# Kernel tuning notes

Measured on AMD Instinct MI355X. Metric: run time of the kernel, lower is better.

The kernel has to match this reference:

```python
import jax, jax.numpy as jnp
import numpy as np

B, Q, N, C = 2, 1024, 4096, 768
H, D, REL = 12, 64, 32
SCALE = 1.0 / np.sqrt(D)


def _lin_coords(n_out, n_in):
    # align_corners=True mapping: x_in = x_out * (n_in-1)/(n_out-1)
    pos = jnp.arange(n_out, dtype=jnp.float32) * ((n_in - 1) / (n_out - 1))
    lo = jnp.clip(jnp.floor(pos).astype(jnp.int32), 0, n_in - 1)
    hi = jnp.clip(lo + 1, 0, n_in - 1)
    w = pos - lo.astype(jnp.float32)
    return lo, hi, w


def _interp_bias(bias, q_len, n_len):
    # bias: [H, 32, 32] -> [H, q_len, n_len] bilinear, align_corners=True
    lq, hq, wq = _lin_coords(q_len, REL)
    ln, hn, wn = _lin_coords(n_len, REL)
    b1 = bias[:, lq, :] * (1.0 - wq)[None, :, None] + bias[:, hq, :] * wq[None, :, None]  # [H,q,32]
    b2 = b1[:, :, ln] * (1.0 - wn)[None, None, :] + b1[:, :, hn] * wn[None, None, :]      # [H,q,n]
    return b2


def setup_inputs() -> dict:
    key = jax.random.key(0)
    ks = jax.random.split(key, 11)
    s = 1.0 / np.sqrt(C)
    return {
        "query": jax.random.normal(ks[0], (B, Q, C), jnp.float32),
        "key_value": jax.random.normal(ks[1], (B, N, C), jnp.float32),
        "Wq": jax.random.normal(ks[2], (C, C), jnp.float32) * s,
        "bq": jax.random.normal(ks[3], (C,), jnp.float32) * 0.01,
        "Wk": jax.random.normal(ks[4], (C, C), jnp.float32) * s,
        "bk": jax.random.normal(ks[5], (C,), jnp.float32) * 0.01,
        "Wv": jax.random.normal(ks[6], (C, C), jnp.float32) * s,
        "bv": jax.random.normal(ks[7], (C,), jnp.float32) * 0.01,
        "Wo": jax.random.normal(ks[8], (C, C), jnp.float32) * s,
        "bo": jax.random.normal(ks[9], (C,), jnp.float32) * 0.01,
        "rel_pos_bias": jax.random.normal(ks[10], (H, REL, REL), jnp.float32) * 0.02,
    }


def reference(query, key_value, Wq, bq, Wk, bk, Wv, bv, Wo, bo, rel_pos_bias):
    b, n, c = key_value.shape
    q_len = query.shape[1]
    # projections (dropout in eval mode -> identity)
    q = (query @ Wq + bq).reshape(b, q_len, H, D).transpose(0, 2, 1, 3)      # [B,H,Q,D]
    k = (key_value @ Wk + bk).reshape(b, n, H, D).transpose(0, 2, 1, 3)      # [B,H,N,D]
    v = (key_value @ Wv + bv).reshape(b, n, H, D).transpose(0, 2, 1, 3)      # [B,H,N,D]
    attn = jnp.einsum('bhqd,bhnd->bhqn', q, k) * SCALE
    attn = attn + _interp_bias(rel_pos_bias, q_len, n)[None]                 # [B,H,Q,N]
    p = jax.nn.softmax(attn, axis=-1)
    out = jnp.einsum('bhqn,bhnd->bhqd', p, v)
    out = out.transpose(0, 2, 1, 3).reshape(b, q_len, c)
    return out @ Wo + bo
```

## Files before the change

kernel.cpp:

```cpp
#include <hip/hip_runtime.h>
#include <stdint.h>

typedef unsigned short ushort_t;
typedef __bf16 bf16x8 __attribute__((ext_vector_type(8)));
typedef float f32x4 __attribute__((ext_vector_type(4)));
typedef unsigned short us4 __attribute__((ext_vector_type(4)));

#define LOG2E 1.4426950408889634f
#define NEG8L (-11.541560327111707f)
#define QSCALE 0.18033688011110974f

__device__ __forceinline__ ushort_t f2b(float f) {
    unsigned u = __float_as_uint(f);
    unsigned r = (u + 0x7fffu + ((u >> 16) & 1u)) >> 16;
    return (ushort_t)r;
}
__device__ __forceinline__ void gld16(const void* g, void* l) {
    __builtin_amdgcn_global_load_lds(
        (__attribute__((address_space(1))) void*)g,
        (__attribute__((address_space(3))) void*)l,
        16, 0, 0);
}

__global__ __launch_bounds__(256) void prep(
        const float* __restrict__ query, const float* __restrict__ keyv,
        const float* __restrict__ Wq, const float* __restrict__ Wk,
        const float* __restrict__ Wv, const float* __restrict__ Wo,
        const float* __restrict__ rel,
        ushort_t* __restrict__ qc, ushort_t* __restrict__ kvc,
        ushort_t* __restrict__ wtq, ushort_t* __restrict__ wtk,
        ushort_t* __restrict__ wtv, ushort_t* __restrict__ wto,
        ushort_t* __restrict__ b1b, ushort_t* __restrict__ wtab) {
    __shared__ ushort_t tsh[32][33];
    const int bid = blockIdx.x, tid = threadIdx.x;
    if (bid < 7680) {
        const float* src = (bid < 1536) ? query : keyv;
        ushort_t* dst = (bid < 1536) ? qc : kvc;
        int i = ((bid < 1536) ? bid : bid - 1536) * 256 + tid;
        float4 x = ((const float4*)src)[i];
        us4 v; v.x = f2b(x.x); v.y = f2b(x.y); v.z = f2b(x.z); v.w = f2b(x.w);
        ((us4*)dst)[i] = v;
    } else if (bid < 9984) {
        int t = bid - 7680, w = t / 576, tt = t - w * 576;
        const float* in = (w == 0) ? Wq : (w == 1) ? Wk : (w == 2) ? Wv : Wo;
        ushort_t* out = (w == 0) ? wtq : (w == 1) ? wtk : (w == 2) ? wtv : wto;
        int x = tid & 31, y = tid >> 5;
        int bx = (tt % 24) * 32, by = (tt / 24) * 32;
#pragma unroll
        for (int j = 0; j < 32; j += 8)
            tsh[y + j][x] = f2b(in[(size_t)(by + y + j) * 768 + bx + x]);
        __syncthreads();
#pragma unroll
        for (int j = 0; j < 32; j += 8)
            out[(size_t)(bx + y + j) * 768 + by + x] = tsh[x][y + j];
    } else if (bid < 11520) {
        int idx = (bid - 9984) * 256 + tid;
        int j = idx & 31, q = (idx >> 5) & 1023, h = idx >> 15;
        float pos = q * (31.0f / 1023.0f);
        float fl = floorf(pos);
        int lo = (int)fl; if (lo > 31) lo = 31;
        float w = pos - fl;
        int hi = lo + 1; if (hi > 31) hi = 31;
        float vlo = rel[(h * 32 + lo) * 32 + j];
        float vhi = rel[(h * 32 + hi) * 32 + j];
        b1b[idx] = f2b((vlo + (vhi - vlo) * w) * LOG2E);
    } else {
        int n = (bid - 11520) * 256 + tid;
        float pos = n * (31.0f / 4095.0f);
        float fl = floorf(pos);
        int ln = (int)fl; if (ln > 31) ln = 31;
        float wn = pos - fl;
        int hn = ln + 1; if (hn > 31) hn = 31;
        float vals[32];
#pragma unroll
        for (int j = 0; j < 32; ++j) vals[j] = 0.f;
        vals[ln] += 1.0f - wn;
        vals[hn] += wn;
#pragma unroll
        for (int j = 0; j < 32; ++j) wtab[n * 32 + j] = f2b(vals[j]);
    }
}

__device__ __forceinline__ void gemm_store(const float* __restrict__ bias,
                                           f32x4 a, void* out,
                                           int mode, int lsh, float scale,
                                           int mbase, int n) {
    if (mode == 2) {
        int h = n >> 6, d = n & 63;
        int b = mbase >> lsh, l = mbase & ((1 << lsh) - 1);
        float bvf = bias[n];
        us4 v;
        v.x = f2b((a[0] + bvf) * scale);
        v.y = f2b((a[1] + bvf) * scale);
        v.z = f2b((a[2] + bvf) * scale);
        v.w = f2b((a[3] + bvf) * scale);
        *(us4*)((ushort_t*)out + ((size_t)((b * 12 + h) * 64 + d) << lsh) + l) = v;
    } else if (mode == 3) {
        int h = mbase >> 6, dbase = mbase & 63;
        int b = n >> lsh, l = n & ((1 << lsh) - 1);
        us4 v;
        v.x = f2b((a[0] + bias[mbase + 0]) * scale);
        v.y = f2b((a[1] + bias[mbase + 1]) * scale);
        v.z = f2b((a[2] + bias[mbase + 2]) * scale);
        v.w = f2b((a[3] + bias[mbase + 3]) * scale);
        *(us4*)((ushort_t*)out + ((((size_t)(b * 12 + h) << lsh) + l) << 6) + dbase) = v;
    } else {
        float4 v;
        v.x = (a[0] + bias[mbase + 0]) * scale;
        v.y = (a[1] + bias[mbase + 1]) * scale;
        v.z = (a[2] + bias[mbase + 2]) * scale;
        v.w = (a[3] + bias[mbase + 3]) * scale;
        *(float4*)((float*)out + (size_t)n * 768 + mbase) = v;
    }
}

__device__ __forceinline__ void gemm_body128(const ushort_t* __restrict__ A,
                                             const ushort_t* __restrict__ Bt,
                                             const float* __restrict__ bias,
                                             void* __restrict__ out,
                                             int mode, int lsh, float scale,
                                             int m0, int n0,
                                             ushort_t* As, ushort_t* Bs, int tid) {
    const int wave = tid >> 6, lane = tid & 63;
    const int quad = lane >> 4, l15 = lane & 15;
    const int wm = wave >> 1, wn = wave & 1;
    const f32x4 z4 = {0.f, 0.f, 0.f, 0.f};
    f32x4 acc[4][4];
#pragma unroll
    for (int i = 0; i < 4; ++i)
#pragma unroll
        for (int j = 0; j < 4; ++j) acc[i][j] = z4;

    const int arow = lane >> 3;
    const int ablk = lane & 7;
    const int kswz = (ablk ^ arow) * 8;

    for (int kk = 0; kk < 768; kk += 64) {
        __syncthreads();
#pragma unroll
        for (int i = 0; i < 4; ++i) {
            int c = wave * 4 + i;
            gld16(A + (size_t)(m0 + c * 8 + arow) * 768 + kk + kswz, (void*)(As + c * 512));
            gld16(Bt + (size_t)(n0 + c * 8 + arow) * 768 + kk + kswz, (void*)(Bs + c * 512));
        }
        __syncthreads();
#pragma unroll
        for (int ks = 0; ks < 2; ++ks) {
            bf16x8 af[4], bf[4];
#pragma unroll
            for (int mb = 0; mb < 4; ++mb) {
                int r = wm * 64 + mb * 16 + l15;
                af[mb] = *(const bf16x8*)(As + r * 64 + (((ks * 4 + quad) ^ (r & 7)) * 8));
            }
#pragma unroll
            for (int nb = 0; nb < 4; ++nb) {
                int r = wn * 64 + nb * 16 + l15;
                bf[nb] = *(const bf16x8*)(Bs + r * 64 + (((ks * 4 + quad) ^ (r & 7)) * 8));
            }
#pragma unroll
            for (int mb = 0; mb < 4; ++mb)
#pragma unroll
                for (int nb = 0; nb < 4; ++nb)
                    acc[mb][nb] = __builtin_amdgcn_mfma_f32_16x16x32_bf16(af[mb], bf[nb], acc[mb][nb], 0, 0, 0);
        }
    }

#pragma unroll
    for (int mb = 0; mb < 4; ++mb) {
        int mbase = m0 + wm * 64 + mb * 16 + quad * 4;
#pragma unroll
        for (int nb = 0; nb < 4; ++nb) {
            int n = n0 + wn * 64 + nb * 16 + l15;
            gemm_store(bias, acc[mb][nb], out, mode, lsh, scale, mbase, n);
        }
    }
}

__device__ __forceinline__ void gemm_body64(const ushort_t* __restrict__ A,
                                            const ushort_t* __restrict__ Bt,
                                            const float* __restrict__ bias,
                                            void* __restrict__ out,
                                            int mode, int lsh, float scale,
                                            int m0, int n0,
                                            ushort_t* As, ushort_t* Bs, int tid) {
    const int wave = tid >> 6, lane = tid & 63;
    const int quad = lane >> 4, l15 = lane & 15;
    const f32x4 z4 = {0.f, 0.f, 0.f, 0.f};
    f32x4 acc[4];
#pragma unroll
    for (int j = 0; j < 4; ++j) acc[j] = z4;

    const int arow = lane >> 3;
    const int ablk = lane & 7;
    const int kswz = (ablk ^ arow) * 8;

    for (int kk = 0; kk < 768; kk += 64) {
        __syncthreads();
#pragma unroll
        for (int i = 0; i < 2; ++i) {
            int c = wave * 2 + i;
            gld16(A + (size_t)(m0 + c * 8 + arow) * 768 + kk + kswz, (void*)(As + c * 512));
            gld16(Bt + (size_t)(n0 + c * 8 + arow) * 768 + kk + kswz, (void*)(Bs + c * 512));
        }
        __syncthreads();
#pragma unroll
        for (int ks = 0; ks < 2; ++ks) {
            bf16x8 af, bf[4];
            {
                int r = wave * 16 + l15;
                af = *(const bf16x8*)(As + r * 64 + (((ks * 4 + quad) ^ (r & 7)) * 8));
            }
#pragma unroll
            for (int nb = 0; nb < 4; ++nb) {
                int r = nb * 16 + l15;
                bf[nb] = *(const bf16x8*)(Bs + r * 64 + (((ks * 4 + quad) ^ (r & 7)) * 8));
            }
#pragma unroll
            for (int nb = 0; nb < 4; ++nb)
                acc[nb] = __builtin_amdgcn_mfma_f32_16x16x32_bf16(af, bf[nb], acc[nb], 0, 0, 0);
        }
    }

    int mbase = m0 + wave * 16 + quad * 4;
#pragma unroll
    for (int nb = 0; nb < 4; ++nb) {
        int n = n0 + nb * 16 + l15;
        gemm_store(bias, acc[nb], out, mode, lsh, scale, mbase, n);
    }
}

__global__ __launch_bounds__(256) void proj3(const ushort_t* __restrict__ qc,
                                             const ushort_t* __restrict__ kvc,
                                             const ushort_t* __restrict__ wtq,
                                             const ushort_t* __restrict__ wtk,
                                             const ushort_t* __restrict__ wtv,
                                             const float* __restrict__ bq,
                                             const float* __restrict__ bk,
                                             const float* __restrict__ bv,
                                             ushort_t* __restrict__ qp,
                                             ushort_t* __restrict__ kp,
                                             ushort_t* __restrict__ vtp) {
    __shared__ __align__(16) ushort_t As[128 * 64];
    __shared__ __align__(16) ushort_t Bs[128 * 64];
    const int bid = blockIdx.x, tid = threadIdx.x;
    if (bid < 96) {
        int t = bid;
        int nt = (t & 7) + 8 * ((t >> 3) & 1), mt = t >> 4;
        gemm_body128(wtq, qc, bq, qp, 3, 10, QSCALE, mt * 128, nt * 128, As, Bs, tid);
    } else if (bid < 480) {
        int t = bid - 96;
        int nt = (t & 7) + 8 * ((t >> 3) & 7), mt = t >> 6;
        gemm_body128(wtk, kvc, bk, kp, 3, 12, 1.0f, mt * 128, nt * 128, As, Bs, tid);
    } else {
        int t = bid - 480, mt = t & 63, nt = t >> 6;
        gemm_body128(kvc, wtv, bv, vtp, 2, 12, 1.0f, mt * 128, nt * 128, As, Bs, tid);
    }
}

__global__ __launch_bounds__(256) void gemm_out(const ushort_t* __restrict__ ab,
                                                const ushort_t* __restrict__ wto,
                                                const float* __restrict__ bo,
                                                float* __restrict__ out) {
    __shared__ __align__(16) ushort_t As[64 * 64];
    __shared__ __align__(16) ushort_t Bs[64 * 64];
    const int bid = blockIdx.x, tid = threadIdx.x;
    int j = bid >> 3;
    int nt = (bid & 7) + 8 * (j & 3), mt = j >> 2;
    gemm_body64(wto, ab, bo, out, 4, 0, 1.0f, mt * 64, nt * 64, As, Bs, tid);
}

__global__ __launch_bounds__(256) void attn64s(const ushort_t* __restrict__ qp,
                                               const ushort_t* __restrict__ kp,
                                               const ushort_t* __restrict__ vt,
                                               const ushort_t* __restrict__ b1b,
                                               const ushort_t* __restrict__ wtab,
                                               float* __restrict__ po,
                                               float* __restrict__ pl,
                                               int sp_base) {
    __shared__ __align__(16) ushort_t k_s[64 * 64];
    __shared__ __align__(16) ushort_t v_s[64 * 64];
    __shared__ __align__(16) float pf[4][576];

    const int tid = threadIdx.x;
    const int wave = tid >> 6, lane = tid & 63;
    const int quad = lane >> 4, l15 = lane & 15;
    const int bid = blockIdx.x;
    const int xcd = bid & 7;
    const int slot = bid >> 3;
    const int g = xcd + 8 * (slot >> 5);
    const int member = slot & 31;
    const int b = g / 12, h = g - b * 12;
    const int qt = member & 15, sp = sp_base + (member >> 4);
    const int q0 = qt * 64;
    const int bh = g;

    const ushort_t* qg = qp + ((size_t)bh * 1024 + q0) * 64;
    const ushort_t* kg = kp + (size_t)bh * 4096 * 64;
    const ushort_t* vg = vt + (size_t)bh * 64 * 4096;

    const int rowq = wave * 16 + l15;
    bf16x8 aq[2];
#pragma unroll
    for (int ks = 0; ks < 2; ++ks)
        aq[ks] = *(const bf16x8*)(qg + (size_t)rowq * 64 + (ks * 4 + quad) * 8);
    bf16x8 ab1 = *(const bf16x8*)(b1b + ((size_t)(h * 1024 + q0 + rowq)) * 32 + quad * 8);

    const f32x4 mC = {NEG8L, NEG8L, NEG8L, NEG8L};
    const f32x4 z4 = {0.f, 0.f, 0.f, 0.f};
    f32x4 o[4];
    float lsum[4];
#pragma unroll
    for (int d = 0; d < 4; ++d) o[d] = z4;
#pragma unroll
    for (int r = 0; r < 4; ++r) lsum[r] = 0.f;

    const int arow = lane >> 3;
    const int ablk = lane & 7;

    for (int nt = 0; nt < 16; ++nt) {
        const int n0 = sp * 1024 + nt * 64;
        __syncthreads();
#pragma unroll
        for (int i = 0; i < 2; ++i) {
            int c = wave * 2 + i;
            int row = c * 8 + arow;
            int k16 = ablk ^ (row & 7);
            gld16(kg + (size_t)(n0 + row) * 64 + k16 * 8, (void*)(k_s + c * 512));
            gld16(vg + (size_t)row * 4096 + n0 + k16 * 8, (void*)(v_s + c * 512));
        }
        __syncthreads();

        bf16x8 wf[4];
#pragma unroll
        for (int nb = 0; nb < 4; ++nb)
            wf[nb] = *(const bf16x8*)(wtab + (size_t)(n0 + nb * 16 + l15) * 32 + quad * 8);

        f32x4 s[4];
#pragma unroll
        for (int nb = 0; nb < 4; ++nb) {
            s[nb] = __builtin_amdgcn_mfma_f32_16x16x32_bf16(ab1, wf[nb], mC, 0, 0, 0);
#pragma unroll
            for (int ks = 0; ks < 2; ++ks) {
                int rn = nb * 16 + l15;
                bf16x8 bk = *(const bf16x8*)(k_s + rn * 64 + (((ks * 4 + quad) ^ (rn & 7)) * 8));
                s[nb] = __builtin_amdgcn_mfma_f32_16x16x32_bf16(aq[ks], bk, s[nb], 0, 0, 0);
            }
        }
#pragma unroll
        for (int nb = 0; nb < 4; ++nb)
#pragma unroll
            for (int r = 0; r < 4; ++r) {
                float p = exp2f(s[nb][r]);
                s[nb][r] = p;
                lsum[r] += p;
            }
#pragma unroll
        for (int p = 0; p < 2; ++p) {
#pragma unroll
            for (int i = 0; i < 2; ++i) {
                int nb = 2 * p + i;
                float* dst = &pf[wave][(i * 16 + l15) * 18 + quad * 4];
                *(float2*)dst = make_float2(s[nb][0], s[nb][1]);
                *(float2*)(dst + 2) = make_float2(s[nb][2], s[nb][3]);
            }
            bf16x8 ap;
#pragma unroll
            for (int j = 0; j < 8; ++j)
                ap[j] = (__bf16)pf[wave][(quad * 8 + j) * 18 + l15];
#pragma unroll
            for (int d = 0; d < 4; ++d) {
                int rd = d * 16 + l15;
                bf16x8 bv = *(const bf16x8*)(v_s + rd * 64 + (((p * 4 + quad) ^ (rd & 7)) * 8));
                o[d] = __builtin_amdgcn_mfma_f32_16x16x32_bf16(ap, bv, o[d], 0, 0, 0);
            }
        }
    }

#pragma unroll
    for (int r = 0; r < 4; ++r)
#pragma unroll
        for (int off = 1; off < 16; off <<= 1)
            lsum[r] += __shfl_xor(lsum[r], off, 64);

    const size_t pbase = ((size_t)(sp * 24 + bh)) * 1024;
#pragma unroll
    for (int r = 0; r < 4; ++r) {
        int qrow = q0 + wave * 16 + quad * 4 + r;
        if (l15 == 0) pl[pbase + qrow] = lsum[r];
#pragma unroll
        for (int d = 0; d < 4; ++d)
            po[(pbase + qrow) * 64 + d * 16 + l15] = o[d][r];
    }
}

__global__ __launch_bounds__(256) void combine(const float* __restrict__ po,
                                               const float* __restrict__ pl,
                                               ushort_t* __restrict__ ab) {
    int idx = blockIdx.x * 256 + threadIdx.x;
    int e = idx * 4;
    int b = e / 786432;
    int rem = e - b * 786432;
    int q = rem / 768;
    int col = rem - q * 768;
    int h = col >> 6, d = col & 63;
    int bh = b * 12 + h;
    float4 acc = {0.f, 0.f, 0.f, 0.f};
    float l = 0.f;
#pragma unroll
    for (int s = 0; s < 4; ++s) {
        size_t base = ((size_t)(s * 24 + bh)) * 1024 + q;
        float4 v = *(const float4*)(po + base * 64 + d);
        acc.x += v.x; acc.y += v.y; acc.z += v.z; acc.w += v.w;
        l += pl[base];
    }
    float inv = 1.0f / l;
    us4 v;
    v.x = f2b(acc.x * inv); v.y = f2b(acc.y * inv);
    v.z = f2b(acc.z * inv); v.w = f2b(acc.w * inv);
    *(us4*)(ab + (size_t)(b * 1024 + q) * 768 + col) = v;
}

extern "C" void kernel_launch(void* const* d_in, const int* in_sizes, int n_in,
                              void* d_out, int out_size, void* d_ws, size_t ws_size,
                              hipStream_t stream) {
    const float* query = (const float*)d_in[0];
    const float* keyv  = (const float*)d_in[1];
    const float* Wq = (const float*)d_in[2];
    const float* bq = (const float*)d_in[3];
    const float* Wk = (const float*)d_in[4];
    const float* bk = (const float*)d_in[5];
    const float* Wv = (const float*)d_in[6];
    const float* bv = (const float*)d_in[7];
    const float* Wo = (const float*)d_in[8];
    const float* bo = (const float*)d_in[9];
    const float* rel = (const float*)d_in[10];

    char* ws = (char*)d_ws;
    ushort_t* qc   = (ushort_t*)(ws + 0);
    ushort_t* kvc  = (ushort_t*)(ws + 3145728);
    ushort_t* wtq  = (ushort_t*)(ws + 15728640);
    ushort_t* wtk  = (ushort_t*)(ws + 16908288);
    ushort_t* wtv  = (ushort_t*)(ws + 18087936);
    ushort_t* wto  = (ushort_t*)(ws + 19267584);
    ushort_t* qp   = (ushort_t*)(ws + 20447232);
    ushort_t* kp   = (ushort_t*)(ws + 23592960);
    ushort_t* vtp  = (ushort_t*)(ws + 36175872);
    ushort_t* b1b  = (ushort_t*)(ws + 48758784);
    ushort_t* wtab = (ushort_t*)(ws + 49545216);
    ushort_t* ab   = (ushort_t*)(ws + 49807360);
    float*    po   = (float*)(ws + 52953088);
    float*    pl   = (float*)(ws + 78118912);

    prep<<<11536, 256, 0, stream>>>(query, keyv, Wq, Wk, Wv, Wo, rel,
                                    qc, kvc, wtq, wtk, wtv, wto, b1b, wtab);
    proj3<<<864, 256, 0, stream>>>(qc, kvc, wtq, wtk, wtv, bq, bk, bv, qp, kp, vtp);
    attn64s<<<768, 256, 0, stream>>>(qp, kp, vtp, b1b, wtab, po, pl, 0);
    attn64s<<<768, 256, 0, stream>>>(qp, kp, vtp, b1b, wtab, po, pl, 2);
    combine<<<1536, 256, 0, stream>>>(po, pl, ab);
    gemm_out<<<384, 256, 0, stream>>>(ab, wto, bo, (float*)d_out);
}
```

Before: 225.1 us.

## Double-buffer GEMM and attention LDS loads; halve KV splits into one launch

The GEMM bodies now use BK=32 tiles in a double-buffered LDS ring. The next tile is issued right after a single barrier, so global-to-LDS loads overlap the MFMAs. The attention kernel likewise double-buffers K/V tiles. It also processes 2048 keys per block (2 splits instead of 4), which merges the two attention launches into one and shrinks the partial buffers that combine reads. Tradeoffs are more LDS per block and possibly lower occupancy. Attention also has fewer blocks in flight per head, each running longer.

After: 231.7 us. 1.03x slower.

```diff
diff --git a/kernel.cpp b/kernel.cpp
--- a/kernel.cpp
+++ b/kernel.cpp
@@ -131,38 +131,42 @@
 #pragma unroll
         for (int j = 0; j < 4; ++j) acc[i][j] = z4;
 
-    const int arow = lane >> 3;
-    const int ablk = lane & 7;
-    const int kswz = (ablk ^ arow) * 8;
-
-    for (int kk = 0; kk < 768; kk += 64) {
+    const int lrow = lane >> 2;
+    const int kswz = ((lane & 3) ^ (lrow & 3)) * 8;
+
+    auto issue = [&](int kk, int buf) {
+#pragma unroll
+        for (int i = 0; i < 2; ++i) {
+            int c = wave * 2 + i;
+            gld16(A + (size_t)(m0 + c * 16 + lrow) * 768 + kk + kswz,
+                  (void*)(As + buf * 4096 + c * 512));
+            gld16(Bt + (size_t)(n0 + c * 16 + lrow) * 768 + kk + kswz,
+                  (void*)(Bs + buf * 4096 + c * 512));
+        }
+    };
+
+    issue(0, 0);
+    for (int it = 0; it < 24; ++it) {
         __syncthreads();
-#pragma unroll
-        for (int i = 0; i < 4; ++i) {
-            int c = wave * 4 + i;
-            gld16(A + (size_t)(m0 + c * 8 + arow) * 768 + kk + kswz, (void*)(As + c * 512));
-            gld16(Bt + (size_t)(n0 + c * 8 + arow) * 768 + kk + kswz, (void*)(Bs + c * 512));
-        }
-        __syncthreads();
-#pragma unroll
-        for (int ks = 0; ks < 2; ++ks) {
-            bf16x8 af[4], bf[4];
-#pragma unroll
-            for (int mb = 0; mb < 4; ++mb) {
-                int r = wm * 64 + mb * 16 + l15;
-                af[mb] = *(const bf16x8*)(As + r * 64 + (((ks * 4 + quad) ^ (r & 7)) * 8));
-            }
-#pragma unroll
-            for (int nb = 0; nb < 4; ++nb) {
-                int r = wn * 64 + nb * 16 + l15;
-                bf[nb] = *(const bf16x8*)(Bs + r * 64 + (((ks * 4 + quad) ^ (r & 7)) * 8));
-            }
-#pragma unroll
-            for (int mb = 0; mb < 4; ++mb)
-#pragma unroll
-                for (int nb = 0; nb < 4; ++nb)
-                    acc[mb][nb] = __builtin_amdgcn_mfma_f32_16x16x32_bf16(af[mb], bf[nb], acc[mb][nb], 0, 0, 0);
-        }
+        if (it + 1 < 24) issue((it + 1) * 32, (it + 1) & 1);
+        const ushort_t* Ab = As + (it & 1) * 4096;
+        const ushort_t* Bb = Bs + (it & 1) * 4096;
+        bf16x8 af[4], bf[4];
+#pragma unroll
+        for (int mb = 0; mb < 4; ++mb) {
+            int r = wm * 64 + mb * 16 + l15;
+            af[mb] = *(const bf16x8*)(Ab + r * 32 + ((quad ^ (r & 3)) * 8));
+        }
+#pragma unroll
+        for (int nb = 0; nb < 4; ++nb) {
+            int r = wn * 64 + nb * 16 + l15;
+            bf[nb] = *(const bf16x8*)(Bb + r * 32 + ((quad ^ (r & 3)) * 8));
+        }
+#pragma unroll
+        for (int mb = 0; mb < 4; ++mb)
+#pragma unroll
+            for (int nb = 0; nb < 4; ++nb)
+                acc[mb][nb] = __builtin_amdgcn_mfma_f32_16x16x32_bf16(af[mb], bf[nb], acc[mb][nb], 0, 0, 0);
     }
 
 #pragma unroll
@@ -190,35 +194,35 @@
 #pragma unroll
     for (int j = 0; j < 4; ++j) acc[j] = z4;
 
-    const int arow = lane >> 3;
-    const int ablk = lane & 7;
-    const int kswz = (ablk ^ arow) * 8;
-
-    for (int kk = 0; kk < 768; kk += 64) {
+    const int lrow = lane >> 2;
+    const int kswz = ((lane & 3) ^ (lrow & 3)) * 8;
+
+    auto issue = [&](int kk, int buf) {
+        gld16(A + (size_t)(m0 + wave * 16 + lrow) * 768 + kk + kswz,
+              (void*)(As + buf * 2048 + wave * 512));
+        gld16(Bt + (size_t)(n0 + wave * 16 + lrow) * 768 + kk + kswz,
+              (void*)(Bs + buf * 2048 + wave * 512));
+    };
+
+    issue(0, 0);
+    for (int it = 0; it < 24; ++it) {
         __syncthreads();
-#pragma unroll
-        for (int i = 0; i < 2; ++i) {
-            int c = wave * 2 + i;
-            gld16(A + (size_t)(m0 + c * 8 + arow) * 768 + kk + kswz, (void*)(As + c * 512));
-            gld16(Bt + (size_t)(n0 + c * 8 + arow) * 768 + kk + kswz, (void*)(Bs + c * 512));
-        }
-        __syncthreads();
-#pragma unroll
-        for (int ks = 0; ks < 2; ++ks) {
-            bf16x8 af, bf[4];
-            {
-                int r = wave * 16 + l15;
-                af = *(const bf16x8*)(As + r * 64 + (((ks * 4 + quad) ^ (r & 7)) * 8));
-            }
-#pragma unroll
-            for (int nb = 0; nb < 4; ++nb) {
-                int r = nb * 16 + l15;
-                bf[nb] = *(const bf16x8*)(Bs + r * 64 + (((ks * 4 + quad) ^ (r & 7)) * 8));
-            }
-#pragma unroll
-            for (int nb = 0; nb < 4; ++nb)
-                acc[nb] = __builtin_amdgcn_mfma_f32_16x16x32_bf16(af, bf[nb], acc[nb], 0, 0, 0);
-        }
+        if (it + 1 < 24) issue((it + 1) * 32, (it + 1) & 1);
+        const ushort_t* Ab = As + (it & 1) * 2048;
+        const ushort_t* Bb = Bs + (it & 1) * 2048;
+        bf16x8 af, bf[4];
+        {
+            int r = wave * 16 + l15;
+            af = *(const bf16x8*)(Ab + r * 32 + ((quad ^ (r & 3)) * 8));
+        }
+#pragma unroll
+        for (int nb = 0; nb < 4; ++nb) {
+            int r = nb * 16 + l15;
+            bf[nb] = *(const bf16x8*)(Bb + r * 32 + ((quad ^ (r & 3)) * 8));
+        }
+#pragma unroll
+        for (int nb = 0; nb < 4; ++nb)
+            acc[nb] = __builtin_amdgcn_mfma_f32_16x16x32_bf16(af, bf[nb], acc[nb], 0, 0, 0);
     }
 
     int mbase = m0 + wave * 16 + quad * 4;
@@ -240,8 +244,8 @@
                                              ushort_t* __restrict__ qp,
                                              ushort_t* __restrict__ kp,
                                              ushort_t* __restrict__ vtp) {
-    __shared__ __align__(16) ushort_t As[128 * 64];
-    __shared__ __align__(16) ushort_t Bs[128 * 64];
+    __shared__ __align__(16) ushort_t As[2 * 128 * 32];
+    __shared__ __align__(16) ushort_t Bs[2 * 128 * 32];
     const int bid = blockIdx.x, tid = threadIdx.x;
     if (bid < 96) {
         int t = bid;
@@ -261,8 +265,8 @@
                                                 const ushort_t* __restrict__ wto,
                                                 const float* __restrict__ bo,
                                                 float* __restrict__ out) {
-    __shared__ __align__(16) ushort_t As[64 * 64];
-    __shared__ __align__(16) ushort_t Bs[64 * 64];
+    __shared__ __align__(16) ushort_t As[2 * 64 * 32];
+    __shared__ __align__(16) ushort_t Bs[2 * 64 * 32];
     const int bid = blockIdx.x, tid = threadIdx.x;
     int j = bid >> 3;
     int nt = (bid & 7) + 8 * (j & 3), mt = j >> 2;
@@ -275,10 +279,9 @@
                                                const ushort_t* __restrict__ b1b,
                                                const ushort_t* __restrict__ wtab,
                                                float* __restrict__ po,
-                                               float* __restrict__ pl,
-                                               int sp_base) {
-    __shared__ __align__(16) ushort_t k_s[64 * 64];
-    __shared__ __align__(16) ushort_t v_s[64 * 64];
+                                               float* __restrict__ pl) {
+    __shared__ __align__(16) ushort_t k_s[2 * 64 * 64];
+    __shared__ __align__(16) ushort_t v_s[2 * 64 * 64];
     __shared__ __align__(16) float pf[4][576];
 
     const int tid = threadIdx.x;
@@ -290,7 +293,7 @@
     const int g = xcd + 8 * (slot >> 5);
     const int member = slot & 31;
     const int b = g / 12, h = g - b * 12;
-    const int qt = member & 15, sp = sp_base + (member >> 4);
+    const int qt = member & 15, sp = member >> 4;
     const int q0 = qt * 64;
     const int bh = g;
 
@@ -316,19 +319,27 @@
 
     const int arow = lane >> 3;
     const int ablk = lane & 7;
-
-    for (int nt = 0; nt < 16; ++nt) {
-        const int n0 = sp * 1024 + nt * 64;
-        __syncthreads();
+    const int nbase = sp * 2048;
+
+    auto issueKV = [&](int nt, int buf) {
+        const int n0 = nbase + nt * 64;
 #pragma unroll
         for (int i = 0; i < 2; ++i) {
             int c = wave * 2 + i;
             int row = c * 8 + arow;
             int k16 = ablk ^ (row & 7);
-            gld16(kg + (size_t)(n0 + row) * 64 + k16 * 8, (void*)(k_s + c * 512));
-            gld16(vg + (size_t)row * 4096 + n0 + k16 * 8, (void*)(v_s + c * 512));
-        }
+            gld16(kg + (size_t)(n0 + row) * 64 + k16 * 8, (void*)(k_s + buf * 4096 + c * 512));
+            gld16(vg + (size_t)row * 4096 + n0 + k16 * 8, (void*)(v_s + buf * 4096 + c * 512));
+        }
+    };
+
+    issueKV(0, 0);
+    for (int nt = 0; nt < 32; ++nt) {
         __syncthreads();
+        if (nt + 1 < 32) issueKV(nt + 1, (nt + 1) & 1);
+        const ushort_t* kb = k_s + (nt & 1) * 4096;
+        const ushort_t* vb = v_s + (nt & 1) * 4096;
+        const int n0 = nbase + nt * 64;
 
         bf16x8 wf[4];
 #pragma unroll
@@ -342,7 +353,7 @@
 #pragma unroll
             for (int ks = 0; ks < 2; ++ks) {
                 int rn = nb * 16 + l15;
-                bf16x8 bk = *(const bf16x8*)(k_s + rn * 64 + (((ks * 4 + quad) ^ (rn & 7)) * 8));
+                bf16x8 bk = *(const bf16x8*)(kb + rn * 64 + (((ks * 4 + quad) ^ (rn & 7)) * 8));
                 s[nb] = __builtin_amdgcn_mfma_f32_16x16x32_bf16(aq[ks], bk, s[nb], 0, 0, 0);
             }
         }
@@ -370,7 +381,7 @@
 #pragma unroll
             for (int d = 0; d < 4; ++d) {
                 int rd = d * 16 + l15;
-                bf16x8 bv = *(const bf16x8*)(v_s + rd * 64 + (((p * 4 + quad) ^ (rd & 7)) * 8));
+                bf16x8 bv = *(const bf16x8*)(vb + rd * 64 + (((p * 4 + quad) ^ (rd & 7)) * 8));
                 o[d] = __builtin_amdgcn_mfma_f32_16x16x32_bf16(ap, bv, o[d], 0, 0, 0);
             }
         }
@@ -407,7 +418,7 @@
     float4 acc = {0.f, 0.f, 0.f, 0.f};
     float l = 0.f;
 #pragma unroll
-    for (int s = 0; s < 4; ++s) {
+    for (int s = 0; s < 2; ++s) {
         size_t base = ((size_t)(s * 24 + bh)) * 1024 + q;
         float4 v = *(const float4*)(po + base * 64 + d);
         acc.x += v.x; acc.y += v.y; acc.z += v.z; acc.w += v.w;
@@ -449,13 +460,12 @@
     ushort_t* wtab = (ushort_t*)(ws + 49545216);
     ushort_t* ab   = (ushort_t*)(ws + 49807360);
     float*    po   = (float*)(ws + 52953088);
-    float*    pl   = (float*)(ws + 78118912);
+    float*    pl   = (float*)(ws + 65536000);
 
     prep<<<11536, 256, 0, stream>>>(query, keyv, Wq, Wk, Wv, Wo, rel,
                                     qc, kvc, wtq, wtk, wtv, wto, b1b, wtab);
     proj3<<<864, 256, 0, stream>>>(qc, kvc, wtq, wtk, wtv, bq, bk, bv, qp, kp, vtp);
-    attn64s<<<768, 256, 0, stream>>>(qp, kp, vtp, b1b, wtab, po, pl, 0);
-    attn64s<<<768, 256, 0, stream>>>(qp, kp, vtp, b1b, wtab, po, pl, 2);
+    attn64s<<<768, 256, 0, stream>>>(qp, kp, vtp, b1b, wtab, po, pl);
     combine<<<1536, 256, 0, stream>>>(po, pl, ab);
     gemm_out<<<384, 256, 0, stream>>>(ab, wto, bo, (float*)d_out);
 }
```

## Transpose attention MFMAs, stage P in bf16, halve KV splits to one launch

Applied to the files above, without the earlier changes.

The attention kernel now computes S transposed by swapping MFMA operands, so each lane holds a query row. P can then be written to LDS directly as packed bf16 instead of going through a float transpose buffer, and the row sum reduces with two shuffles. The KV split count drops from 4 to 2, with each block covering 2048 keys in a single launch, which removes one kernel launch and halves the partial-output traffic read by combine. The wtab load is also moved before the barrier. The trade-off is fewer concurrent blocks (768 total instead of 1536) with longer serial loops, which may reduce latency hiding.

After: 218.4 us. 3.0% less time.

```diff
diff --git a/kernel.cpp b/kernel.cpp
--- a/kernel.cpp
+++ b/kernel.cpp
@@ -3,6 +3,7 @@
 
 typedef unsigned short ushort_t;
 typedef __bf16 bf16x8 __attribute__((ext_vector_type(8)));
+typedef __bf16 bf16x4v __attribute__((ext_vector_type(4)));
 typedef float f32x4 __attribute__((ext_vector_type(4)));
 typedef unsigned short us4 __attribute__((ext_vector_type(4)));
 
@@ -275,11 +276,10 @@
                                                const ushort_t* __restrict__ b1b,
                                                const ushort_t* __restrict__ wtab,
                                                float* __restrict__ po,
-                                               float* __restrict__ pl,
-                                               int sp_base) {
+                                               float* __restrict__ pl) {
     __shared__ __align__(16) ushort_t k_s[64 * 64];
     __shared__ __align__(16) ushort_t v_s[64 * 64];
-    __shared__ __align__(16) float pf[4][576];
+    __shared__ __align__(16) __bf16 pB[4][16 * 72];
 
     const int tid = threadIdx.x;
     const int wave = tid >> 6, lane = tid & 63;
@@ -290,7 +290,7 @@
     const int g = xcd + 8 * (slot >> 5);
     const int member = slot & 31;
     const int b = g / 12, h = g - b * 12;
-    const int qt = member & 15, sp = sp_base + (member >> 4);
+    const int qt = member & 15, sp = member >> 4;
     const int q0 = qt * 64;
     const int bh = g;
 
@@ -308,17 +308,17 @@
     const f32x4 mC = {NEG8L, NEG8L, NEG8L, NEG8L};
     const f32x4 z4 = {0.f, 0.f, 0.f, 0.f};
     f32x4 o[4];
-    float lsum[4];
+    float lsum = 0.f;
 #pragma unroll
     for (int d = 0; d < 4; ++d) o[d] = z4;
-#pragma unroll
-    for (int r = 0; r < 4; ++r) lsum[r] = 0.f;
 
     const int arow = lane >> 3;
     const int ablk = lane & 7;
-
-    for (int nt = 0; nt < 16; ++nt) {
-        const int n0 = sp * 1024 + nt * 64;
+    const int nbase = sp * 2048;
+    __bf16* pw = &pB[wave][0];
+
+    for (int nt = 0; nt < 32; ++nt) {
+        const int n0 = nbase + nt * 64;
         __syncthreads();
 #pragma unroll
         for (int i = 0; i < 2; ++i) {
@@ -328,69 +328,55 @@
             gld16(kg + (size_t)(n0 + row) * 64 + k16 * 8, (void*)(k_s + c * 512));
             gld16(vg + (size_t)row * 4096 + n0 + k16 * 8, (void*)(v_s + c * 512));
         }
-        __syncthreads();
-
         bf16x8 wf[4];
 #pragma unroll
         for (int nb = 0; nb < 4; ++nb)
             wf[nb] = *(const bf16x8*)(wtab + (size_t)(n0 + nb * 16 + l15) * 32 + quad * 8);
+        __syncthreads();
 
         f32x4 s[4];
 #pragma unroll
         for (int nb = 0; nb < 4; ++nb) {
-            s[nb] = __builtin_amdgcn_mfma_f32_16x16x32_bf16(ab1, wf[nb], mC, 0, 0, 0);
+            s[nb] = __builtin_amdgcn_mfma_f32_16x16x32_bf16(wf[nb], ab1, mC, 0, 0, 0);
 #pragma unroll
             for (int ks = 0; ks < 2; ++ks) {
                 int rn = nb * 16 + l15;
                 bf16x8 bk = *(const bf16x8*)(k_s + rn * 64 + (((ks * 4 + quad) ^ (rn & 7)) * 8));
-                s[nb] = __builtin_amdgcn_mfma_f32_16x16x32_bf16(aq[ks], bk, s[nb], 0, 0, 0);
-            }
-        }
-#pragma unroll
-        for (int nb = 0; nb < 4; ++nb)
+                s[nb] = __builtin_amdgcn_mfma_f32_16x16x32_bf16(bk, aq[ks], s[nb], 0, 0, 0);
+            }
+        }
+#pragma unroll
+        for (int nb = 0; nb < 4; ++nb) {
+            bf16x4v pv;
 #pragma unroll
             for (int r = 0; r < 4; ++r) {
                 float p = exp2f(s[nb][r]);
-                s[nb][r] = p;
-                lsum[r] += p;
-            }
-#pragma unroll
-        for (int p = 0; p < 2; ++p) {
-#pragma unroll
-            for (int i = 0; i < 2; ++i) {
-                int nb = 2 * p + i;
-                float* dst = &pf[wave][(i * 16 + l15) * 18 + quad * 4];
-                *(float2*)dst = make_float2(s[nb][0], s[nb][1]);
-                *(float2*)(dst + 2) = make_float2(s[nb][2], s[nb][3]);
-            }
-            bf16x8 ap;
-#pragma unroll
-            for (int j = 0; j < 8; ++j)
-                ap[j] = (__bf16)pf[wave][(quad * 8 + j) * 18 + l15];
-#pragma unroll
-            for (int d = 0; d < 4; ++d) {
-                int rd = d * 16 + l15;
-                bf16x8 bv = *(const bf16x8*)(v_s + rd * 64 + (((p * 4 + quad) ^ (rd & 7)) * 8));
-                o[d] = __builtin_amdgcn_mfma_f32_16x16x32_bf16(ap, bv, o[d], 0, 0, 0);
-            }
-        }
-    }
-
-#pragma unroll
-    for (int r = 0; r < 4; ++r)
-#pragma unroll
-        for (int off = 1; off < 16; off <<= 1)
-            lsum[r] += __shfl_xor(lsum[r], off, 64);
+                lsum += p;
+                pv[r] = (__bf16)p;
+            }
+            *(bf16x4v*)(pw + l15 * 72 + nb * 16 + quad * 4) = pv;
+        }
+#pragma unroll
+        for (int ks = 0; ks < 2; ++ks) {
+            bf16x8 bp = *(const bf16x8*)(pw + l15 * 72 + ks * 32 + quad * 8);
+#pragma unroll
+            for (int dt = 0; dt < 4; ++dt) {
+                int rd = dt * 16 + l15;
+                bf16x8 av = *(const bf16x8*)(v_s + rd * 64 + (((ks * 4 + quad) ^ (rd & 7)) * 8));
+                o[dt] = __builtin_amdgcn_mfma_f32_16x16x32_bf16(av, bp, o[dt], 0, 0, 0);
+            }
+        }
+    }
+
+    lsum += __shfl_xor(lsum, 16, 64);
+    lsum += __shfl_xor(lsum, 32, 64);
 
     const size_t pbase = ((size_t)(sp * 24 + bh)) * 1024;
-#pragma unroll
-    for (int r = 0; r < 4; ++r) {
-        int qrow = q0 + wave * 16 + quad * 4 + r;
-        if (l15 == 0) pl[pbase + qrow] = lsum[r];
-#pragma unroll
-        for (int d = 0; d < 4; ++d)
-            po[(pbase + qrow) * 64 + d * 16 + l15] = o[d][r];
-    }
+    const int qrow = q0 + wave * 16 + l15;
+    if (lane < 16) pl[pbase + qrow] = lsum;
+#pragma unroll
+    for (int dt = 0; dt < 4; ++dt)
+        *(float4*)(po + (pbase + qrow) * 64 + dt * 16 + quad * 4) = (float4){o[dt][0], o[dt][1], o[dt][2], o[dt][3]};
 }
 
 __global__ __launch_bounds__(256) void combine(const float* __restrict__ po,
@@ -407,7 +393,7 @@
     float4 acc = {0.f, 0.f, 0.f, 0.f};
     float l = 0.f;
 #pragma unroll
-    for (int s = 0; s < 4; ++s) {
+    for (int s = 0; s < 2; ++s) {
         size_t base = ((size_t)(s * 24 + bh)) * 1024 + q;
         float4 v = *(const float4*)(po + base * 64 + d);
         acc.x += v.x; acc.y += v.y; acc.z += v.z; acc.w += v.w;
@@ -449,13 +435,12 @@
     ushort_t* wtab = (ushort_t*)(ws + 49545216);
     ushort_t* ab   = (ushort_t*)(ws + 49807360);
     float*    po   = (float*)(ws + 52953088);
-    float*    pl   = (float*)(ws + 78118912);
+    float*    pl   = (float*)(ws + 65536000);
 
     prep<<<11536, 256, 0, stream>>>(query, keyv, Wq, Wk, Wv, Wo, rel,
                                     qc, kvc, wtq, wtk, wtv, wto, b1b, wtab);
     proj3<<<864, 256, 0, stream>>>(qc, kvc, wtq, wtk, wtv, bq, bk, bv, qp, kp, vtp);
-    attn64s<<<768, 256, 0, stream>>>(qp, kp, vtp, b1b, wtab, po, pl, 0);
-    attn64s<<<768, 256, 0, stream>>>(qp, kp, vtp, b1b, wtab, po, pl, 2);
+    attn64s<<<768, 256, 0, stream>>>(qp, kp, vtp, b1b, wtab, po, pl);
     combine<<<1536, 256, 0, stream>>>(po, pl, ab);
     gemm_out<<<384, 256, 0, stream>>>(ab, wto, bo, (float*)d_out);
 }
```
